# Kernel tuning notes

Hardware: AMD Instinct MI355X
Metric: run time of the kernel (lower is better)

The kernel has to match this reference:

```python
import jax, jax.numpy as jnp
import numpy as np

N_ITEMS = 50000; LM_IN = 768; D = 128; B = 256; L = 50
NH = 2; NL = 2; FF = 4 * D
TEMP = 0.1; BETA1 = 0.5; BETA2 = 0.5
NEG = -1e9


def _ln(x, g, b, eps=1e-5):
    m = x.mean(-1, keepdims=True)
    v = ((x - m) ** 2).mean(-1, keepdims=True)
    return (x - m) / jnp.sqrt(v + eps) * g + b


def _encoder(h, mask, P):
    # SASRec/BERT-style TransformerEncoder: pos-emb + LN, then NL blocks of
    # causal+padding-masked MHA and GELU FFN with post-LN residuals.
    pos, ln0g, ln0b, Wqkv, bqkv, Wo, bo, l1g, l1b, W1, b1, W2, b2, l2g, l2b = P
    Bh, Lh, Dh = h.shape
    dh = Dh // NH
    keep = jnp.tril(jnp.broadcast_to((mask != 0)[:, None, None, :], (Bh, 1, Lh, Lh)))
    bias = jnp.where(keep, 0.0, NEG)  # additive attention mask, [B,1,L,L]
    h = _ln(h + pos, ln0g, ln0b)
    scale = float(1.0 / np.sqrt(dh))
    for l in range(NL):
        qkv = h @ Wqkv[l] + bqkv[l]
        q, k, v = jnp.split(qkv, 3, axis=-1)
        sp = lambda t: t.reshape(Bh, Lh, NH, dh).transpose(0, 2, 1, 3)
        q, k, v = sp(q), sp(k), sp(v)
        att = jax.nn.softmax(jnp.einsum('bhqd,bhkd->bhqk', q, k) * scale + bias, axis=-1)
        o = jnp.einsum('bhqk,bhkd->bhqd', att, v).transpose(0, 2, 1, 3).reshape(Bh, Lh, Dh)
        h = _ln(h + o @ Wo[l] + bo[l], l1g[l], l1b[l])
        f = jax.nn.gelu(h @ W1[l] + b1[l]) @ W2[l] + b2[l]
        h = _ln(h + f, l2g[l], l2b[l])
    return h


def _last(trans, mask):
    # gather embedding at the last valid position: index = mask.sum(1) - 1
    idx = mask.sum(1).astype(jnp.int32) - 1
    return jnp.take_along_axis(trans, idx[:, None, None], axis=1)[:, 0]


def setup_inputs():
    key = jax.random.key(0)
    ks = jax.random.split(key, 32)
    s = 0.02

    def p(i, shape):
        return jax.random.normal(ks[i], shape, jnp.float32) * s

    inp = {}
    inp['x'] = jax.random.normal(ks[0], (N_ITEMS, LM_IN), jnp.float32)
    inp['uid'] = jax.random.randint(ks[1], (B,), 0, 100000)
    inp['edge_index'] = jax.random.randint(ks[2], (2, 1000), 0, N_ITEMS)
    inp['max_itemid'] = N_ITEMS - 1
    inp['itemid'] = jax.random.randint(ks[3], (B, L), 0, N_ITEMS)
    inp['mask'] = jnp.ones((B, L), jnp.float32)
    inp['id_emb'] = p(4, (N_ITEMS, D))
    inp['id_ln_g'] = jnp.ones(D); inp['id_ln_b'] = jnp.zeros(D)
    inp['text_W'] = p(5, (LM_IN, D)); inp['text_b'] = jnp.zeros(D)
    inp['text_ln_g'] = jnp.ones(D); inp['text_ln_b'] = jnp.zeros(D)
    for pre, base in (('ide_', 6), ('te_', 16)):
        inp[pre + 'pos'] = p(base, (L, D))
        inp[pre + 'ln0_g'] = jnp.ones(D); inp[pre + 'ln0_b'] = jnp.zeros(D)
        inp[pre + 'Wqkv'] = p(base + 1, (NL, D, 3 * D)); inp[pre + 'bqkv'] = jnp.zeros((NL, 3 * D))
        inp[pre + 'Wo'] = p(base + 2, (NL, D, D)); inp[pre + 'bo'] = jnp.zeros((NL, D))
        inp[pre + 'ln1_g'] = jnp.ones((NL, D)); inp[pre + 'ln1_b'] = jnp.zeros((NL, D))
        inp[pre + 'W1'] = p(base + 3, (NL, D, FF)); inp[pre + 'b1'] = jnp.zeros((NL, FF))
        inp[pre + 'W2'] = p(base + 4, (NL, FF, D)); inp[pre + 'b2'] = jnp.zeros((NL, D))
        inp[pre + 'ln2_g'] = jnp.ones((NL, D)); inp[pre + 'ln2_b'] = jnp.zeros((NL, D))
    return inp


def reference(x, uid, edge_index, max_itemid, itemid, mask,
              id_emb, id_ln_g, id_ln_b, text_W, text_b, text_ln_g, text_ln_b,
              ide_pos, ide_ln0_g, ide_ln0_b, ide_Wqkv, ide_bqkv, ide_Wo, ide_bo,
              ide_ln1_g, ide_ln1_b, ide_W1, ide_b1, ide_W2, ide_b2, ide_ln2_g, ide_ln2_b,
              te_pos, te_ln0_g, te_ln0_b, te_Wqkv, te_bqkv, te_Wo, te_bo,
              te_ln1_g, te_ln1_b, te_W1, te_b1, te_W2, te_b2, te_ln2_g, te_ln2_b):
    # --- ID module: layernorm over the full embedding table, gather, encode ---
    gnn_emb = _ln(id_emb, id_ln_g, id_ln_b)  # [n_items, D]
    ideP = (ide_pos, ide_ln0_g, ide_ln0_b, ide_Wqkv, ide_bqkv, ide_Wo, ide_bo,
            ide_ln1_g, ide_ln1_b, ide_W1, ide_b1, ide_W2, ide_b2, ide_ln2_g, ide_ln2_b)
    trans = _encoder(gnn_emb[itemid], mask, ideP)  # [B,L,D]
    session_emb = _last(trans, mask)  # [B,D]
    item_embs = gnn_emb[:max_itemid + 1]
    scores1 = session_emb @ item_embs.T  # [B, n_items]
    # --- Text module: linear+relu (dropout off at eval), layernorm, encode ---
    xmap = _ln(jax.nn.relu(x @ text_W + text_b), text_ln_g, text_ln_b)  # [n_items, D]
    teP = (te_pos, te_ln0_g, te_ln0_b, te_Wqkv, te_bqkv, te_Wo, te_bo,
           te_ln1_g, te_ln1_b, te_W1, te_b1, te_W2, te_b2, te_ln2_g, te_ln2_b)
    trans2 = _encoder(xmap[itemid], mask, teP)
    session_feat = _last(trans2, mask)
    scores2 = (session_feat @ xmap[:max_itemid + 1].T) / TEMP
    # eval path: combined score
    scores = BETA1 * scores1 + BETA2 * scores2
    return (scores, scores1, scores2, item_embs, gnn_emb[:max_itemid + 1], xmap[:max_itemid + 1])
```

## Files before the change

### kernel.cpp

```cpp
#include <hip/hip_runtime.h>

#define DEV __device__ __forceinline__

typedef float f32x4 __attribute__((ext_vector_type(4)));
typedef __bf16 bf16x8 __attribute__((ext_vector_type(8)));
#define MFMA16(a,b,c) __builtin_amdgcn_mfma_f32_16x16x32_bf16(a,b,c,0,0,0)

#define ASTRIDE 136
#define QSTRIDE 72
#define PSTRIDE 132

DEV float wsum(float v){
  #pragma unroll
  for (int o = 32; o > 0; o >>= 1) v += __shfl_xor(v, o, 64);
  return v;
}

DEV float gelu_f(float x){
  float u = 0.7978845608028654f * (x + 0.044715f * x * x * x);
  float e = __expf(2.f * u);
  float th = 1.f - 2.f / (e + 1.f);
  return 0.5f * x * (1.f + th);
}

__global__ __launch_bounds__(256) void ln_kernel(const float* in,
    float* out0, float* out1,
    const float* __restrict__ g, const float* __restrict__ bb, int nrows)
{
  int w = threadIdx.x >> 6, l = threadIdx.x & 63;
  int row = blockIdx.x * 4 + w;
  if (row >= nrows) return;
  const float* rp = in + (size_t)row * 128;
  float v0 = rp[l], v1 = rp[l + 64];
  float m = wsum(v0 + v1) * 0.0078125f;
  float d0 = v0 - m, d1 = v1 - m;
  float var = wsum(d0 * d0 + d1 * d1) * 0.0078125f;
  float rs = rsqrtf(var + 1e-5f);
  float o0 = d0 * rs * g[l] + bb[l];
  float o1 = d1 * rs * g[l + 64] + bb[l + 64];
  size_t base = (size_t)row * 128;
  out0[base + l] = o0; out0[base + l + 64] = o1;
  if (out1){ out1[base + l] = o0; out1[base + l + 64] = o1; }
}

__global__ __launch_bounds__(256) void prep_w(
    const float* __restrict__ Wa, const float* __restrict__ Wb,
    __bf16* __restrict__ dst, int K, int N, int nmat)
{
  int tid = blockIdx.x * 256 + threadIdx.x;
  int tpm = (N >> 4) * (K >> 5);
  if (tid >= nmat * tpm * 64) return;
  int lane = tid & 63;
  int tile = (tid >> 6) % tpm;
  int mat  = tid / (tpm * 64);
  const float* W;
  if (nmat == 1) W = Wa;
  else W = ((mat >> 1) ? Wb : Wa) + (size_t)(mat & 1) * K * N;
  int kdiv = K >> 5;
  int nt = tile / kdiv, kt = tile - nt * kdiv;
  int col  = nt * 16 + (lane & 15);
  int krow = kt * 32 + (lane >> 4) * 8;
  __bf16 v[8];
  #pragma unroll
  for (int j = 0; j < 8; j++) v[j] = (__bf16)W[(size_t)(krow + j) * N + col];
  *(bf16x8*)(dst + (size_t)tid * 8) = *(bf16x8*)v;
}

__global__ __launch_bounds__(256) void xmap_mfma(
    const float* __restrict__ X, const __bf16* __restrict__ wt,
    const float* __restrict__ bias, float* __restrict__ out)
{
  __shared__ __bf16 xb[64 * ASTRIDE];
  const int t = threadIdx.x, w = t >> 6, l = t & 63, lm = l & 15, quad = l >> 4;
  const int r0 = blockIdx.x * 64;
  f32x4 acc[8];
  #pragma unroll
  for (int nt = 0; nt < 8; nt++) acc[nt] = (f32x4){0.f,0.f,0.f,0.f};
  for (int kc = 0; kc < 6; kc++){
    for (int i = t; i < 64 * 32; i += 256){
      int r = i >> 5, c4 = (i & 31) * 4;
      float4 v = make_float4(0.f,0.f,0.f,0.f);
      if (r0 + r < 50000) v = *(const float4*)&X[(size_t)(r0 + r) * 768 + kc * 128 + c4];
      xb[r*ASTRIDE + c4 + 0] = (__bf16)v.x;
      xb[r*ASTRIDE + c4 + 1] = (__bf16)v.y;
      xb[r*ASTRIDE + c4 + 2] = (__bf16)v.z;
      xb[r*ASTRIDE + c4 + 3] = (__bf16)v.w;
    }
    __syncthreads();
    bf16x8 af[4];
    #pragma unroll
    for (int kt = 0; kt < 4; kt++)
      af[kt] = *(const bf16x8*)&xb[(w*16 + lm)*ASTRIDE + kt*32 + quad*8];
    #pragma unroll
    for (int nt = 0; nt < 8; nt++)
      #pragma unroll
      for (int kt = 0; kt < 4; kt++)
        acc[nt] = MFMA16(af[kt], *(const bf16x8*)(wt + ((size_t)(nt*24 + kc*4 + kt)*64 + l)*8), acc[nt]);
    __syncthreads();
  }
  #pragma unroll
  for (int nt = 0; nt < 8; nt++){
    int n = nt*16 + lm;
    float bs = bias[n];
    #pragma unroll
    for (int r = 0; r < 4; r++){
      int row = r0 + w*16 + quad*4 + r;
      if (row < 50000) out[(size_t)row*128 + n] = fmaxf(acc[nt][r] + bs, 0.f);
    }
  }
}

struct EncP {
  const float *pos, *ln0g, *ln0b, *bqkv, *bo, *ln1g, *ln1b, *b1, *b2, *ln2g, *ln2b;
  const __bf16 *wq, *wo, *w1, *w2;
  const float* emb;
  float* outT;
};

DEV void ln_reg(float res[8][4], const float* g, const float* bb, int lm){
  float gv[8], bv[8];
  #pragma unroll
  for (int nt = 0; nt < 8; nt++){ gv[nt] = g[nt*16 + lm]; bv[nt] = bb[nt*16 + lm]; }
  #pragma unroll
  for (int r = 0; r < 4; r++){
    float s = 0.f;
    #pragma unroll
    for (int nt = 0; nt < 8; nt++) s += res[nt][r];
    s += __shfl_xor(s, 1, 64); s += __shfl_xor(s, 2, 64);
    s += __shfl_xor(s, 4, 64); s += __shfl_xor(s, 8, 64);
    float mean = s * 0.0078125f;
    float v = 0.f;
    #pragma unroll
    for (int nt = 0; nt < 8; nt++){ float d = res[nt][r] - mean; v += d * d; }
    v += __shfl_xor(v, 1, 64); v += __shfl_xor(v, 2, 64);
    v += __shfl_xor(v, 4, 64); v += __shfl_xor(v, 8, 64);
    float rs = rsqrtf(v * 0.0078125f + 1e-5f);
    #pragma unroll
    for (int nt = 0; nt < 8; nt++)
      res[nt][r] = (res[nt][r] - mean) * rs * gv[nt] + bv[nt];
  }
}

DEV void stage_res(const float res[8][4], __bf16* ab, int mb, int quad, int lm){
  #pragma unroll
  for (int r = 0; r < 4; r++){
    int m = mb + quad*4 + r;
    #pragma unroll
    for (int nt = 0; nt < 8; nt++)
      ab[m*ASTRIDE + nt*16 + lm] = (__bf16)res[nt][r];
  }
}

__global__ __launch_bounds__(256, 2) void encoder_mfma(
    EncP P0, EncP P1, const int* __restrict__ itemid, const float* __restrict__ mask)
{
  EncP P = (blockIdx.x < 256) ? P0 : P1;
  const int b = blockIdx.x & 255;
  const int t = threadIdx.x, w = t >> 6, l = t & 63;
  const int lm = l & 15, quad = l >> 4;
  const int mb = w * 16;
  const int am = mb + lm;

  __shared__ __align__(16) char pool[72704];
  __bf16* ab   = (__bf16*)pool;
  __bf16* qbuf = (__bf16*)(pool + 17408);
  __bf16* kb   = (__bf16*)(pool + 35840);
  __bf16* vb   = (__bf16*)(pool + 54272);
  float*  hfp  = (float*)pool;
  __shared__ float maskv[64];

  if (t < 64) maskv[t] = (t < 50) ? mask[b*50 + t] : 0.f;

  for (int r = w; r < 50; r += 4){
    int it = itemid[b*50 + r];
    const float* er = P.emb + (size_t)it * 128;
    float v0 = er[l]      + P.pos[r*128 + l];
    float v1 = er[l + 64] + P.pos[r*128 + l + 64];
    float m = wsum(v0 + v1) * 0.0078125f;
    float d0 = v0 - m, d1 = v1 - m;
    float var = wsum(d0*d0 + d1*d1) * 0.0078125f;
    float rs = rsqrtf(var + 1e-5f);
    hfp[r*PSTRIDE + l]      = d0 * rs * P.ln0g[l] + P.ln0b[l];
    hfp[r*PSTRIDE + l + 64] = d1 * rs * P.ln0g[l + 64] + P.ln0b[l + 64];
  }
  __syncthreads();

  float res[8][4];
  #pragma unroll
  for (int r = 0; r < 4; r++){
    int m = mb + quad*4 + r;
    #pragma unroll
    for (int nt = 0; nt < 8; nt++)
      res[nt][r] = (m < 50) ? hfp[m*PSTRIDE + nt*16 + lm] : 0.f;
  }

  for (int lay = 0; lay < 2; ++lay){
    const __bf16* wq = P.wq + lay * 49152;
    const __bf16* wo = P.wo + lay * 16384;
    const __bf16* w1 = P.w1 + lay * 65536;
    const __bf16* w2 = P.w2 + lay * 65536;
    const float* bq  = P.bqkv + lay * 384;
    const float* bo  = P.bo   + lay * 128;
    const float* g1  = P.ln1g + lay * 128;
    const float* b1n = P.ln1b + lay * 128;
    const float* b1f = P.b1   + lay * 512;
    const float* b2f = P.b2   + lay * 128;
    const float* g2  = P.ln2g + lay * 128;
    const float* b2n = P.ln2b + lay * 128;

    __syncthreads();

    stage_res(res, ab, mb, quad, lm);
    bf16x8 afh[4];
    #pragma unroll
    for (int kt = 0; kt < 4; kt++)
      afh[kt] = *(const bf16x8*)&ab[am*ASTRIDE + kt*32 + quad*8];

    #pragma unroll
    for (int nt = 0; nt < 24; nt++){
      f32x4 acc = (f32x4){0.f,0.f,0.f,0.f};
      #pragma unroll
      for (int kt = 0; kt < 4; kt++)
        acc = MFMA16(afh[kt], *(const bf16x8*)(wq + ((size_t)(nt*4 + kt)*64 + l)*8), acc);
      int n = nt*16 + lm;
      float bias = bq[n];
      int part = n >> 7, hd = (n >> 6) & 1, d = n & 63;
      __bf16* q_ = qbuf + hd*64*QSTRIDE;
      __bf16* k_ = kb   + hd*64*QSTRIDE;
      __bf16* v_ = vb   + hd*64*QSTRIDE;
      #pragma unroll
      for (int r = 0; r < 4; r++){
        int m = mb + quad*4 + r;
        float v = acc[r] + bias;
        if (part == 0)      q_[m*QSTRIDE + d] = (__bf16)v;
        else if (part == 1) k_[m*QSTRIDE + d] = (__bf16)v;
        else                v_[d*QSTRIDE + m] = (__bf16)v;
      }
    }
    __syncthreads();

    #pragma unroll
    for (int hd = 0; hd < 2; hd++){
      __bf16* q_ = qbuf + hd*64*QSTRIDE;
      const __bf16* k_ = kb + hd*64*QSTRIDE;
      const __bf16* v_ = vb + hd*64*QSTRIDE;
      bf16x8 aq0 = *(const bf16x8*)&q_[am*QSTRIDE + quad*8];
      bf16x8 aq1 = *(const bf16x8*)&q_[am*QSTRIDE + 32 + quad*8];
      f32x4 sf[4];
      #pragma unroll
      for (int nt = 0; nt < 4; nt++){
        f32x4 acc = (f32x4){0.f,0.f,0.f,0.f};
        acc = MFMA16(aq0, *(const bf16x8*)&k_[(nt*16 + lm)*QSTRIDE + quad*8], acc);
        acc = MFMA16(aq1, *(const bf16x8*)&k_[(nt*16 + lm)*QSTRIDE + 32 + quad*8], acc);
        sf[nt] = acc;
      }
      #pragma unroll
      for (int r = 0; r < 4; r++){
        int q = mb + quad*4 + r;
        float sv[4];
        float mx = -3e38f;
        #pragma unroll
        for (int nt = 0; nt < 4; nt++){
          int ki = nt*16 + lm;
          float s = sf[nt][r] * 0.125f;
          bool keep = (ki <= q) && (maskv[ki] != 0.f);
          s = keep ? s : -1e9f;
          sv[nt] = s; mx = fmaxf(mx, s);
        }
        #pragma unroll
        for (int o = 1; o < 16; o <<= 1) mx = fmaxf(mx, __shfl_xor(mx, o, 64));
        float sum = 0.f;
        #pragma unroll
        for (int nt = 0; nt < 4; nt++){ float p = __expf(sv[nt] - mx); sv[nt] = p; sum += p; }
        #pragma unroll
        for (int o = 1; o < 16; o <<= 1) sum += __shfl_xor(sum, o, 64);
        float inv = 1.f / sum;
        #pragma unroll
        for (int nt = 0; nt < 4; nt++)
          q_[q*QSTRIDE + nt*16 + lm] = (__bf16)(sv[nt] * inv);
      }
      bf16x8 ap0 = *(const bf16x8*)&q_[am*QSTRIDE + quad*8];
      bf16x8 ap1 = *(const bf16x8*)&q_[am*QSTRIDE + 32 + quad*8];
      #pragma unroll
      for (int nt = 0; nt < 4; nt++){
        f32x4 acc = (f32x4){0.f,0.f,0.f,0.f};
        acc = MFMA16(ap0, *(const bf16x8*)&v_[(nt*16 + lm)*QSTRIDE + quad*8], acc);
        acc = MFMA16(ap1, *(const bf16x8*)&v_[(nt*16 + lm)*QSTRIDE + 32 + quad*8], acc);
        int dcol = hd*64 + nt*16 + lm;
        #pragma unroll
        for (int r = 0; r < 4; r++)
          ab[(mb + quad*4 + r)*ASTRIDE + dcol] = (__bf16)acc[r];
      }
    }

    {
      bf16x8 af[4];
      #pragma unroll
      for (int kt = 0; kt < 4; kt++)
        af[kt] = *(const bf16x8*)&ab[am*ASTRIDE + kt*32 + quad*8];
      #pragma unroll
      for (int nt = 0; nt < 8; nt++){
        f32x4 acc = (f32x4){0.f,0.f,0.f,0.f};
        #pragma unroll
        for (int kt = 0; kt < 4; kt++)
          acc = MFMA16(af[kt], *(const bf16x8*)(wo + ((size_t)(nt*4 + kt)*64 + l)*8), acc);
        float bias = bo[nt*16 + lm];
        #pragma unroll
        for (int r = 0; r < 4; r++)
          res[nt][r] += acc[r] + bias;
      }
    }
    ln_reg(res, g1, b1n, lm);

    stage_res(res, ab, mb, quad, lm);
    {
      bf16x8 ah[4];
      #pragma unroll
      for (int kt = 0; kt < 4; kt++)
        ah[kt] = *(const bf16x8*)&ab[am*ASTRIDE + kt*32 + quad*8];
      f32x4 acc2[8];
      #pragma unroll
      for (int nt = 0; nt < 8; nt++) acc2[nt] = (f32x4){0.f,0.f,0.f,0.f};
      for (int ch = 0; ch < 4; ch++){
        #pragma unroll
        for (int nt = 0; nt < 8; nt++){
          f32x4 acc = (f32x4){0.f,0.f,0.f,0.f};
          #pragma unroll
          for (int kt = 0; kt < 4; kt++)
            acc = MFMA16(ah[kt], *(const bf16x8*)(w1 + ((size_t)((ch*8 + nt)*4 + kt)*64 + l)*8), acc);
          float bias = b1f[ch*128 + nt*16 + lm];
          #pragma unroll
          for (int r = 0; r < 4; r++)
            ab[(mb + quad*4 + r)*ASTRIDE + nt*16 + lm] = (__bf16)gelu_f(acc[r] + bias);
        }
        bf16x8 a2[4];
        #pragma unroll
        for (int kt = 0; kt < 4; kt++)
          a2[kt] = *(const bf16x8*)&ab[am*ASTRIDE + kt*32 + quad*8];
        #pragma unroll
        for (int nt = 0; nt < 8; nt++)
          #pragma unroll
          for (int kt = 0; kt < 4; kt++)
            acc2[nt] = MFMA16(a2[kt], *(const bf16x8*)(w2 + ((size_t)(nt*16 + ch*4 + kt)*64 + l)*8), acc2[nt]);
      }
      #pragma unroll
      for (int nt = 0; nt < 8; nt++){
        float bias = b2f[nt*16 + lm];
        #pragma unroll
        for (int r = 0; r < 4; r++)
          res[nt][r] += acc2[nt][r] + bias;
      }
    }
    ln_reg(res, g2, b2n, lm);
  }

  {
    float sm = 0.f;
    for (int i = 0; i < 50; i++) sm += maskv[i];
    int idx = min(49, max(0, (int)sm - 1));
    #pragma unroll
    for (int r = 0; r < 4; r++){
      if (mb + quad*4 + r == idx){
        #pragma unroll
        for (int nt = 0; nt < 8; nt++)
          P.outT[(nt*16 + lm)*256 + b] = res[nt][r];
      }
    }
  }
}

__global__ __launch_bounds__(256) void scores_kernel(
    const float* __restrict__ seT, const float* __restrict__ sfT,
    const float* __restrict__ ie,  const float* __restrict__ xm,
    float* __restrict__ sc, float* __restrict__ s1, float* __restrict__ s2)
{
  __shared__ float iet[16 * 128];
  __shared__ float xmt[16 * 128];
  const int t = threadIdx.x;
  const size_t j0 = (size_t)blockIdx.x * 16;
  {
    const float4* ig = (const float4*)(ie + j0 * 128);
    const float4* xg = (const float4*)(xm + j0 * 128);
    float4* a = (float4*)iet; float4* c4 = (float4*)xmt;
    for (int i = t; i < 512; i += 256){ a[i] = ig[i]; c4[i] = xg[i]; }
  }
  __syncthreads();
  float a1[16], a2[16];
  #pragma unroll
  for (int j = 0; j < 16; j++){ a1[j] = 0.f; a2[j] = 0.f; }
  for (int k = 0; k < 128; k += 4){
    float se0 = seT[(k+0)*256 + t], se1 = seT[(k+1)*256 + t];
    float se2 = seT[(k+2)*256 + t], se3 = seT[(k+3)*256 + t];
    float sf0 = sfT[(k+0)*256 + t], sf1 = sfT[(k+1)*256 + t];
    float sf2 = sfT[(k+2)*256 + t], sf3 = sfT[(k+3)*256 + t];
    #pragma unroll
    for (int j = 0; j < 16; j++){
      float4 iv = *(const float4*)&iet[j*128 + k];
      float4 xv = *(const float4*)&xmt[j*128 + k];
      a1[j] += iv.x*se0 + iv.y*se1 + iv.z*se2 + iv.w*se3;
      a2[j] += xv.x*sf0 + xv.y*sf1 + xv.z*sf2 + xv.w*sf3;
    }
  }
  size_t rb = (size_t)t * 50000 + j0;
  #pragma unroll
  for (int j = 0; j < 16; j += 4){
    float4 v1 = make_float4(a1[j], a1[j+1], a1[j+2], a1[j+3]);
    float4 v2 = make_float4(a2[j]*10.f, a2[j+1]*10.f, a2[j+2]*10.f, a2[j+3]*10.f);
    float4 vs = make_float4(0.5f*(v1.x+v2.x), 0.5f*(v1.y+v2.y),
                            0.5f*(v1.z+v2.z), 0.5f*(v1.w+v2.w));
    *(float4*)&s1[rb + j] = v1;
    *(float4*)&s2[rb + j] = v2;
    *(float4*)&sc[rb + j] = vs;
  }
}

extern "C" void kernel_launch(void* const* d_in, const int* in_sizes, int n_in,
                              void* d_out, int out_size, void* d_ws, size_t ws_size,
                              hipStream_t stream)
{
  const float* x       = (const float*)d_in[0];
  const int*   itemid  = (const int*)d_in[4];
  const float* mask    = (const float*)d_in[5];
  const float* id_emb  = (const float*)d_in[6];
  const float* id_g    = (const float*)d_in[7];
  const float* id_b    = (const float*)d_in[8];
  const float* text_W  = (const float*)d_in[9];
  const float* text_b  = (const float*)d_in[10];
  const float* text_g  = (const float*)d_in[11];
  const float* text_bb = (const float*)d_in[12];

  float* out = (float*)d_out;
  float* o_scores = out;
  float* o_s1     = out + 12800000;
  float* o_s2     = out + 25600000;
  float* o_item   = out + 38400000;
  float* o_gnn    = out + 44800000;
  float* o_xmap   = out + 51200000;

  float* seT = (float*)d_ws;
  float* sfT = seT + 32768;
  __bf16* wp   = (__bf16*)((char*)d_ws + 262144);
  __bf16* wqkv = wp;
  __bf16* wo   = wp + 196608;
  __bf16* w1p  = wp + 262144;
  __bf16* w2p  = wp + 524288;
  __bf16* wtx  = wp + 786432;

  prep_w<<<96, 256, 0, stream>>>((const float*)d_in[16], (const float*)d_in[31], wqkv, 128, 384, 4);
  prep_w<<<32, 256, 0, stream>>>((const float*)d_in[18], (const float*)d_in[33], wo,   128, 128, 4);
  prep_w<<<128,256, 0, stream>>>((const float*)d_in[22], (const float*)d_in[37], w1p,  128, 512, 4);
  prep_w<<<128,256, 0, stream>>>((const float*)d_in[24], (const float*)d_in[39], w2p,  512, 128, 4);
  prep_w<<<48, 256, 0, stream>>>(text_W, text_W, wtx, 768, 128, 1);

  ln_kernel<<<12500, 256, 0, stream>>>(id_emb, o_item, o_gnn, id_g, id_b, 50000);
  xmap_mfma<<<782, 256, 0, stream>>>(x, wtx, text_b, o_xmap);
  ln_kernel<<<12500, 256, 0, stream>>>(o_xmap, o_xmap, nullptr, text_g, text_bb, 50000);

  EncP P0, P1;
  P0.pos = (const float*)d_in[13]; P0.ln0g = (const float*)d_in[14]; P0.ln0b = (const float*)d_in[15];
  P0.bqkv = (const float*)d_in[17]; P0.bo = (const float*)d_in[19];
  P0.ln1g = (const float*)d_in[20]; P0.ln1b = (const float*)d_in[21];
  P0.b1 = (const float*)d_in[23]; P0.b2 = (const float*)d_in[25];
  P0.ln2g = (const float*)d_in[26]; P0.ln2b = (const float*)d_in[27];
  P0.wq = wqkv; P0.wo = wo; P0.w1 = w1p; P0.w2 = w2p;
  P0.emb = o_item; P0.outT = seT;

  P1.pos = (const float*)d_in[28]; P1.ln0g = (const float*)d_in[29]; P1.ln0b = (const float*)d_in[30];
  P1.bqkv = (const float*)d_in[32]; P1.bo = (const float*)d_in[34];
  P1.ln1g = (const float*)d_in[35]; P1.ln1b = (const float*)d_in[36];
  P1.b1 = (const float*)d_in[38]; P1.b2 = (const float*)d_in[40];
  P1.ln2g = (const float*)d_in[41]; P1.ln2b = (const float*)d_in[42];
  P1.wq = wqkv + 2*49152; P1.wo = wo + 2*16384; P1.w1 = w1p + 2*65536; P1.w2 = w2p + 2*65536;
  P1.emb = o_xmap; P1.outT = sfT;

  encoder_mfma<<<512, 256, 0, stream>>>(P0, P1, itemid, mask);

  scores_kernel<<<3125, 256, 0, stream>>>(seT, sfT, o_item, o_xmap,
                                          o_scores, o_s1, o_s2);
}
```

Before: 832.7 us.

## Compute final score matrices with bf16 MFMA using pre-packed item fragments

Replaces the scalar FP32 scores kernel with a bf16 MFMA kernel that tiles 64 sessions by 128 items per block. Item embedding tables are first converted into MFMA-fragment-ordered bf16 buffers in the workspace by a new prep kernel. Results are staged through shared memory so the three score outputs are written with coalesced float4 stores. This trades FP32 precision of the score dot products for bf16 inputs and adds two extra conversion passes over the item tables.

```diff
diff --git a/kernel.cpp b/kernel.cpp
--- a/kernel.cpp
+++ b/kernel.cpp
@@ -9,6 +9,7 @@
 #define ASTRIDE 136
 #define QSTRIDE 72
 #define PSTRIDE 132
+#define CSTRIDE 132
 
 DEV float wsum(float v){
   #pragma unroll
@@ -66,6 +67,19 @@
   *(bf16x8*)(dst + (size_t)tid * 8) = *(bf16x8*)v;
 }
 
+__global__ __launch_bounds__(256) void prep_items(
+    const float* __restrict__ src, __bf16* __restrict__ dst)
+{
+  int tid = blockIdx.x * 256 + threadIdx.x;
+  int lane = tid & 63, kt = (tid >> 6) & 3, nt = tid >> 8;
+  if (nt >= 3125) return;
+  const float* p = src + (size_t)(nt*16 + (lane & 15))*128 + kt*32 + (lane >> 4)*8;
+  float4 v0 = *(const float4*)p, v1 = *(const float4*)(p + 4);
+  __bf16 v[8] = {(__bf16)v0.x,(__bf16)v0.y,(__bf16)v0.z,(__bf16)v0.w,
+                 (__bf16)v1.x,(__bf16)v1.y,(__bf16)v1.z,(__bf16)v1.w};
+  *(bf16x8*)(dst + (size_t)tid * 8) = *(bf16x8*)v;
+}
+
 __global__ __launch_bounds__(256) void xmap_mfma(
     const float* __restrict__ X, const __bf16* __restrict__ wt,
     const float* __restrict__ bias, float* __restrict__ out)
@@ -369,48 +383,93 @@
   }
 }
 
-__global__ __launch_bounds__(256) void scores_kernel(
+__global__ __launch_bounds__(256, 2) void scores_mfma(
     const float* __restrict__ seT, const float* __restrict__ sfT,
-    const float* __restrict__ ie,  const float* __restrict__ xm,
+    const __bf16* __restrict__ ieF, const __bf16* __restrict__ xmF,
     float* __restrict__ sc, float* __restrict__ s1, float* __restrict__ s2)
 {
-  __shared__ float iet[16 * 128];
-  __shared__ float xmt[16 * 128];
-  const int t = threadIdx.x;
-  const size_t j0 = (size_t)blockIdx.x * 16;
-  {
-    const float4* ig = (const float4*)(ie + j0 * 128);
-    const float4* xg = (const float4*)(xm + j0 * 128);
-    float4* a = (float4*)iet; float4* c4 = (float4*)xmt;
-    for (int i = t; i < 512; i += 256){ a[i] = ig[i]; c4[i] = xg[i]; }
+  __shared__ __bf16 Ase[64 * ASTRIDE];
+  __shared__ __bf16 Asf[64 * ASTRIDE];
+  __shared__ float  Cst[64 * CSTRIDE];
+  const int t = threadIdx.x, w = t >> 6, l = t & 63;
+  const int lm = l & 15, quad = l >> 4;
+  const int ic = blockIdx.x % 391;
+  const int sg = blockIdx.x / 391;
+  const int s0 = sg * 64;
+  const size_t j0 = (size_t)ic * 128;
+  const int ncols = (ic < 390) ? 128 : 80;
+  const int ntmax = (ncols + 15) >> 4;
+
+  for (int i = t; i < 64 * 128; i += 256){
+    int k = i >> 6, s = i & 63;
+    Ase[s*ASTRIDE + k] = (__bf16)seT[k*256 + s0 + s];
+    Asf[s*ASTRIDE + k] = (__bf16)sfT[k*256 + s0 + s];
   }
   __syncthreads();
-  float a1[16], a2[16];
-  #pragma unroll
-  for (int j = 0; j < 16; j++){ a1[j] = 0.f; a2[j] = 0.f; }
-  for (int k = 0; k < 128; k += 4){
-    float se0 = seT[(k+0)*256 + t], se1 = seT[(k+1)*256 + t];
-    float se2 = seT[(k+2)*256 + t], se3 = seT[(k+3)*256 + t];
-    float sf0 = sfT[(k+0)*256 + t], sf1 = sfT[(k+1)*256 + t];
-    float sf2 = sfT[(k+2)*256 + t], sf3 = sfT[(k+3)*256 + t];
-    #pragma unroll
-    for (int j = 0; j < 16; j++){
-      float4 iv = *(const float4*)&iet[j*128 + k];
-      float4 xv = *(const float4*)&xmt[j*128 + k];
-      a1[j] += iv.x*se0 + iv.y*se1 + iv.z*se2 + iv.w*se3;
-      a2[j] += xv.x*sf0 + xv.y*sf1 + xv.z*sf2 + xv.w*sf3;
-    }
-  }
-  size_t rb = (size_t)t * 50000 + j0;
-  #pragma unroll
-  for (int j = 0; j < 16; j += 4){
-    float4 v1 = make_float4(a1[j], a1[j+1], a1[j+2], a1[j+3]);
-    float4 v2 = make_float4(a2[j]*10.f, a2[j+1]*10.f, a2[j+2]*10.f, a2[j+3]*10.f);
-    float4 vs = make_float4(0.5f*(v1.x+v2.x), 0.5f*(v1.y+v2.y),
-                            0.5f*(v1.z+v2.z), 0.5f*(v1.w+v2.w));
-    *(float4*)&s1[rb + j] = v1;
-    *(float4*)&s2[rb + j] = v2;
-    *(float4*)&sc[rb + j] = vs;
+
+  bf16x8 a1f[4], a2f[4];
+  #pragma unroll
+  for (int kt = 0; kt < 4; kt++){
+    a1f[kt] = *(const bf16x8*)&Ase[(w*16 + lm)*ASTRIDE + kt*32 + quad*8];
+    a2f[kt] = *(const bf16x8*)&Asf[(w*16 + lm)*ASTRIDE + kt*32 + quad*8];
+  }
+  f32x4 acc1[8], acc2[8];
+  #pragma unroll
+  for (int nt = 0; nt < 8; nt++){
+    acc1[nt] = (f32x4){0.f,0.f,0.f,0.f};
+    acc2[nt] = (f32x4){0.f,0.f,0.f,0.f};
+  }
+  for (int nt = 0; nt < ntmax; nt++){
+    size_t ntg = (size_t)ic*8 + nt;
+    #pragma unroll
+    for (int kt = 0; kt < 4; kt++){
+      acc1[nt] = MFMA16(a1f[kt], *(const bf16x8*)(ieF + ((ntg*4 + kt)*64 + l)*8), acc1[nt]);
+      acc2[nt] = MFMA16(a2f[kt], *(const bf16x8*)(xmF + ((ntg*4 + kt)*64 + l)*8), acc2[nt]);
+    }
+  }
+
+  #pragma unroll
+  for (int nt = 0; nt < 8; nt++){
+    if (nt < ntmax){
+      #pragma unroll
+      for (int r = 0; r < 4; r++)
+        Cst[(w*16 + quad*4 + r)*CSTRIDE + nt*16 + lm] = acc1[nt][r];
+    }
+  }
+  __syncthreads();
+  float4 r1[8];
+  #pragma unroll
+  for (int i = 0; i < 8; i++){
+    int idx = i*256 + t;
+    int row = idx >> 5, c4 = idx & 31;
+    r1[i] = *(const float4*)&Cst[row*CSTRIDE + c4*4];
+    if (c4*4 < ncols)
+      *(float4*)&s1[(size_t)(s0 + row)*50000 + j0 + c4*4] = r1[i];
+  }
+  __syncthreads();
+
+  #pragma unroll
+  for (int nt = 0; nt < 8; nt++){
+    if (nt < ntmax){
+      #pragma unroll
+      for (int r = 0; r < 4; r++)
+        Cst[(w*16 + quad*4 + r)*CSTRIDE + nt*16 + lm] = acc2[nt][r];
+    }
+  }
+  __syncthreads();
+  #pragma unroll
+  for (int i = 0; i < 8; i++){
+    int idx = i*256 + t;
+    int row = idx >> 5, c4 = idx & 31;
+    if (c4*4 < ncols){
+      float4 v2 = *(const float4*)&Cst[row*CSTRIDE + c4*4];
+      v2.x *= 10.f; v2.y *= 10.f; v2.z *= 10.f; v2.w *= 10.f;
+      float4 vs = make_float4(0.5f*(r1[i].x + v2.x), 0.5f*(r1[i].y + v2.y),
+                              0.5f*(r1[i].z + v2.z), 0.5f*(r1[i].w + v2.w));
+      size_t base = (size_t)(s0 + row)*50000 + j0 + c4*4;
+      *(float4*)&s2[base] = v2;
+      *(float4*)&sc[base] = vs;
+    }
   }
 }
 
@@ -445,6 +504,8 @@
   __bf16* w1p  = wp + 262144;
   __bf16* w2p  = wp + 524288;
   __bf16* wtx  = wp + 786432;
+  __bf16* ieF  = (__bf16*)((char*)d_ws + 2097152);
+  __bf16* xmF  = (__bf16*)((char*)d_ws + 14897152);
 
   prep_w<<<96, 256, 0, stream>>>((const float*)d_in[16], (const float*)d_in[31], wqkv, 128, 384, 4);
   prep_w<<<32, 256, 0, stream>>>((const float*)d_in[18], (const float*)d_in[33], wo,   128, 128, 4);
@@ -453,8 +514,10 @@
   prep_w<<<48, 256, 0, stream>>>(text_W, text_W, wtx, 768, 128, 1);
 
   ln_kernel<<<12500, 256, 0, stream>>>(id_emb, o_item, o_gnn, id_g, id_b, 50000);
+  prep_items<<<3125, 256, 0, stream>>>(o_item, ieF);
   xmap_mfma<<<782, 256, 0, stream>>>(x, wtx, text_b, o_xmap);
   ln_kernel<<<12500, 256, 0, stream>>>(o_xmap, o_xmap, nullptr, text_g, text_bb, 50000);
+  prep_items<<<3125, 256, 0, stream>>>(o_xmap, xmF);
 
   EncP P0, P1;
   P0.pos = (const float*)d_in[13]; P0.ln0g = (const float*)d_in[14]; P0.ln0b = (const float*)d_in[15];
@@ -475,6 +538,6 @@
 
   encoder_mfma<<<512, 256, 0, stream>>>(P0, P1, itemid, mask);
 
-  scores_kernel<<<3125, 256, 0, stream>>>(seT, sfT, o_item, o_xmap,
-                                          o_scores, o_s1, o_s2);
-}
+  scores_mfma<<<1564, 256, 0, stream>>>(seT, sfT, ieF, xmF,
+                                        o_scores, o_s1, o_s2);
+}
```

After: 825.8 us. Within noise of the previous version (-0.8%).
